# Kernel optimization log

Hardware: AMD Instinct MI355X
Metric: run time of the kernel (lower is better)

## Reference

```python
import jax, jax.numpy as jnp
import numpy as np

DIM = 512
HEAD_DIM = 32
NUM_HEADS = DIM // HEAD_DIM
SCALE = HEAD_DIM ** -0.5


def setup_inputs() -> dict:
    key = jax.random.key(0)
    k1, k2, k3 = jax.random.split(key, 3)
    B, H, W, C = 8, 32, 32, DIM
    x = jax.random.normal(k1, (B, H, W, C), dtype=jnp.float32)
    w_qkv = jax.random.normal(k2, (C, 3 * C), dtype=jnp.float32) * (C ** -0.5)
    w_proj = jax.random.normal(k3, (C, C), dtype=jnp.float32) * (C ** -0.5)
    b_proj = jnp.zeros((C,), dtype=jnp.float32)
    return {"x": x, "w_qkv": w_qkv, "w_proj": w_proj, "b_proj": b_proj}


def reference(x, w_qkv, w_proj, b_proj):
    B, H, W, C = x.shape
    N = H * W
    xt = x.reshape(B, N, C)
    qkv = xt @ w_qkv                       # [B, N, 3C]
    qkv = qkv.reshape(B, N, 3, NUM_HEADS, HEAD_DIM)
    qkv = jnp.transpose(qkv, (2, 0, 3, 1, 4))  # [3, B, heads, N, head_dim]
    q, k, v = qkv[0], qkv[1], qkv[2]
    attn = jnp.einsum('bhid,bhjd->bhij', q * SCALE, k)  # [B, heads, N, N]
    attn = jax.nn.softmax(attn, axis=-1)
    out = jnp.einsum('bhij,bhjd->bhid', attn, v)        # [B, heads, N, head_dim]
    out = jnp.transpose(out, (0, 2, 1, 3)).reshape(B, N, C)
    out = out @ w_proj + b_proj
    return out.reshape(B, H, W, C)
```

## Files before the change

### kernel.cpp

```cpp
#include <hip/hip_runtime.h>
#include <hip/hip_bf16.h>

typedef __bf16 bf16x8 __attribute__((ext_vector_type(8)));
typedef float  f32x4  __attribute__((ext_vector_type(4)));
typedef float  f32x16 __attribute__((ext_vector_type(16)));

#define NB 8
#define NTOK 1024
#define CDIM 512
#define NHEAD 16
#define HDIM 32
#define ATT_SCALE 0.17677669529663687f
#define LOG2E 1.4426950408889634f
#define QSCALE2 (ATT_SCALE * LOG2E)
#define NEGM2 (-12.0f * LOG2E)

struct __align__(8) bf4pack { __hip_bfloat16 x, y, z, w; };

__global__ __launch_bounds__(256)
void k_f32_to_bf16(const float* __restrict__ in, __hip_bfloat16* __restrict__ out, int n4) {
  int i = blockIdx.x * blockDim.x + threadIdx.x;
  if (i >= n4) return;
  float4 v = reinterpret_cast<const float4*>(in)[i];
  bf4pack o{__float2bfloat16(v.x), __float2bfloat16(v.y),
            __float2bfloat16(v.z), __float2bfloat16(v.w)};
  reinterpret_cast<bf4pack*>(out)[i] = o;
}

__global__ __launch_bounds__(256)
void k_transpose_bf16(const float* __restrict__ w, __hip_bfloat16* __restrict__ wt,
                      int K, int N) {
  __shared__ float tile[32][33];
  const int n0 = blockIdx.x * 32, k0 = blockIdx.y * 32;
  const int tx = threadIdx.x, ty = threadIdx.y;
  #pragma unroll
  for (int r = ty; r < 32; r += 8) tile[r][tx] = w[(size_t)(k0 + r) * N + n0 + tx];
  __syncthreads();
  #pragma unroll
  for (int r = ty; r < 32; r += 8)
    wt[(size_t)(n0 + r) * K + k0 + tx] = __float2bfloat16(tile[tx][r]);
}

__device__ __forceinline__ void gload_lds16(const void* g, void* l) {
  __builtin_amdgcn_global_load_lds(
      (const __attribute__((address_space(1))) unsigned int*)g,
      (__attribute__((address_space(3))) unsigned int*)l, 16, 0, 0);
}

template <int MODE>
__global__ __launch_bounds__(256, 2)
void gemm128(const __hip_bfloat16* __restrict__ A,
             const __hip_bfloat16* __restrict__ Bt,
             __hip_bfloat16* __restrict__ Qb,
             __hip_bfloat16* __restrict__ Kb,
             __hip_bfloat16* __restrict__ Vtb,
             float* __restrict__ outF,
             const float* __restrict__ bias,
             int mtiles, int ntiles) {
  __shared__ __hip_bfloat16 As[2][128 * 32];
  __shared__ __hip_bfloat16 Bs[2][128 * 32];

  const int t = threadIdx.x;
  const int wid = t >> 6, lane = t & 63;
  const int wr = wid >> 1, wc = wid & 1;
  const int lrow = lane & 15, lk8 = (lane >> 4) * 8;

  const int bid = blockIdx.x;
  const int chunk = (mtiles * ntiles) >> 3;
  const int wg = (bid & 7) * chunk + (bid >> 3);
  const int bm = (wg / ntiles) * 128;
  const int bn = (wg % ntiles) * 128;

  const bool swapped = (MODE == 0) && (bn >= 1024);

  const f32x4 fzero = {0.f, 0.f, 0.f, 0.f};
  f32x4 acc[4][4];
  #pragma unroll
  for (int m = 0; m < 4; ++m)
    #pragma unroll
    for (int n = 0; n < 4; ++n) acc[m][n] = fzero;

  auto stage = [&](int buf, int kt) {
    #pragma unroll
    for (int p = 0; p < 2; ++p) {
      const int c = p * 256 + t;
      const int row = c >> 2;
      const int kof = (c & 3) * 8;
      gload_lds16(A + (size_t)(bm + row) * CDIM + kt * 32 + kof,
                  &As[buf][(p * 256 + (t >> 6) * 64) * 8]);
      gload_lds16(Bt + (size_t)(bn + row) * CDIM + kt * 32 + kof,
                  &Bs[buf][(p * 256 + (t >> 6) * 64) * 8]);
    }
  };

  stage(0, 0);
  const int NKT = CDIM / 32;
  for (int kt = 0; kt < NKT; ++kt) {
    __syncthreads();
    if (kt + 1 < NKT) stage((kt + 1) & 1, kt + 1);
    const int bi = kt & 1;
    bf16x8 af[4], bfv[4];
    #pragma unroll
    for (int m = 0; m < 4; ++m)
      af[m] = *reinterpret_cast<const bf16x8*>(&As[bi][(wr * 64 + m * 16 + lrow) * 32 + lk8]);
    #pragma unroll
    for (int n = 0; n < 4; ++n)
      bfv[n] = *reinterpret_cast<const bf16x8*>(&Bs[bi][(wc * 64 + n * 16 + lrow) * 32 + lk8]);
    if (swapped) {
      #pragma unroll
      for (int m = 0; m < 4; ++m)
        #pragma unroll
        for (int n = 0; n < 4; ++n)
          acc[m][n] = __builtin_amdgcn_mfma_f32_16x16x32_bf16(bfv[n], af[m], acc[m][n], 0, 0, 0);
    } else {
      #pragma unroll
      for (int m = 0; m < 4; ++m)
        #pragma unroll
        for (int n = 0; n < 4; ++n)
          acc[m][n] = __builtin_amdgcn_mfma_f32_16x16x32_bf16(af[m], bfv[n], acc[m][n], 0, 0, 0);
    }
  }

  if constexpr (MODE == 0) {
    if (swapped) {
      #pragma unroll
      for (int m = 0; m < 4; ++m) {
        #pragma unroll
        for (int n = 0; n < 4; ++n) {
          #pragma unroll
          for (int i = 0; i < 4; ++i) {
            const int gn = bn + wc * 64 + n * 16 + (lane >> 4) * 4 + i;
            const int gm = bm + wr * 64 + m * 16 + lrow;
            const int r = gn & 511;
            const int h = r >> 5, d = r & 31;
            const int b = gm >> 10, tok = gm & 1023;
            const int ph = b * NHEAD + h;
            Vtb[((size_t)ph * HDIM + d) * NTOK + tok] = __float2bfloat16(acc[m][n][i]);
          }
        }
      }
    } else {
      #pragma unroll
      for (int m = 0; m < 4; ++m) {
        #pragma unroll
        for (int n = 0; n < 4; ++n) {
          #pragma unroll
          for (int i = 0; i < 4; ++i) {
            const int gm = bm + wr * 64 + m * 16 + (lane >> 4) * 4 + i;
            const int gn = bn + wc * 64 + n * 16 + lrow;
            const float v = acc[m][n][i];
            const int which = gn >> 9;
            const int r = gn & 511;
            const int h = r >> 5, d = r & 31;
            const int b = gm >> 10, tok = gm & 1023;
            const int ph = b * NHEAD + h;
            if (which == 0)
              Qb[((size_t)ph * NTOK + tok) * HDIM + d] = __float2bfloat16(v * QSCALE2);
            else
              Kb[((size_t)ph * NTOK + tok) * HDIM + d] = __float2bfloat16(v);
          }
        }
      }
    }
  } else {
    #pragma unroll
    for (int m = 0; m < 4; ++m) {
      #pragma unroll
      for (int n = 0; n < 4; ++n) {
        #pragma unroll
        for (int i = 0; i < 4; ++i) {
          const int gm = bm + wr * 64 + m * 16 + (lane >> 4) * 4 + i;
          const int gn = bn + wc * 64 + n * 16 + lrow;
          outF[(size_t)gm * CDIM + gn] = acc[m][n][i] + bias[gn];
        }
      }
    }
  }
}

__device__ __forceinline__ unsigned pk2(float a, float b) {
  union { __hip_bfloat16 h; unsigned short u; } x, y;
  x.h = __float2bfloat16(a); y.h = __float2bfloat16(b);
  return (unsigned)x.u | ((unsigned)y.u << 16);
}

union B32x4 { unsigned u[4]; bf16x8 v; };

__global__ __launch_bounds__(256)
void k_attn(const __hip_bfloat16* __restrict__ Q,
            const __hip_bfloat16* __restrict__ K,
            const __hip_bfloat16* __restrict__ Vt,
            __hip_bfloat16* __restrict__ out) {
  const int wid = threadIdx.x >> 6, lane = threadIdx.x & 63;
  const int pair = blockIdx.x & 127;
  const int qblk = blockIdx.x >> 7;
  const int b = pair >> 4, h = pair & 15;
  const int q0 = qblk * 128 + wid * 32;
  const int lq = lane & 31, hi = lane >> 5;

  const size_t pb = (size_t)pair * NTOK * HDIM;
  const bf16x8 qf0 = *reinterpret_cast<const bf16x8*>(&Q[pb + (size_t)(q0 + lq) * HDIM + hi * 8]);
  const bf16x8 qf1 = *reinterpret_cast<const bf16x8*>(&Q[pb + (size_t)(q0 + lq) * HDIM + 16 + hi * 8]);

  f32x16 o;
  #pragma unroll
  for (int r = 0; r < 16; ++r) o[r] = 0.f;
  float l_r = 0.f;

  const __hip_bfloat16* Kp = &K[pb + (size_t)lq * HDIM + hi * 8];
  const __hip_bfloat16* Vp = &Vt[(size_t)pair * HDIM * NTOK + (size_t)lq * NTOK + hi * 8];

  for (int t = 0; t < 32; ++t) {
    const __hip_bfloat16* kb = Kp + (size_t)t * 32 * HDIM;
    const bf16x8 kf0 = *reinterpret_cast<const bf16x8*>(kb);
    const bf16x8 kf1 = *reinterpret_cast<const bf16x8*>(kb + 16);
    f32x16 s;
    #pragma unroll
    for (int r = 0; r < 16; ++r) s[r] = NEGM2;
    s = __builtin_amdgcn_mfma_f32_32x32x16_bf16(kf0, qf0, s, 0, 0, 0);
    s = __builtin_amdgcn_mfma_f32_32x32x16_bf16(kf1, qf1, s, 0, 0, 0);

    float p[16];
    float ts = 0.f;
    #pragma unroll
    for (int r = 0; r < 16; ++r) { p[r] = __builtin_amdgcn_exp2f(s[r]); ts += p[r]; }
    ts += __shfl_xor(ts, 32, 64);
    l_r += ts;

    #pragma unroll
    for (int ks = 0; ks < 2; ++ks) {
      const int r0 = 8 * ks;
      const bf16x8 vf = *reinterpret_cast<const bf16x8*>(Vp + t * 32 + ks * 16);
      const unsigned pA = pk2(p[r0 + 0], p[r0 + 1]);
      const unsigned pB = pk2(p[r0 + 2], p[r0 + 3]);
      const unsigned pC = pk2(p[r0 + 4], p[r0 + 5]);
      const unsigned pD = pk2(p[r0 + 6], p[r0 + 7]);
      const unsigned sA = hi ? pA : pC;
      const unsigned sB = hi ? pB : pD;
      const unsigned rA = (unsigned)__shfl_xor((int)sA, 32, 64);
      const unsigned rB = (unsigned)__shfl_xor((int)sB, 32, 64);
      B32x4 f;
      f.u[0] = hi ? rA : pA;
      f.u[1] = hi ? rB : pB;
      f.u[2] = hi ? pC : rA;
      f.u[3] = hi ? pD : rB;
      o = __builtin_amdgcn_mfma_f32_32x32x16_bf16(vf, f.v, o, 0, 0, 0);
    }
  }

  const float rinv = 1.0f / l_r;
  __hip_bfloat16* orow = &out[((size_t)b * NTOK + q0 + lq) * CDIM + h * HDIM];
  #pragma unroll
  for (int g = 0; g < 4; ++g) {
    bf4pack w;
    w.x = __float2bfloat16(o[4 * g + 0] * rinv);
    w.y = __float2bfloat16(o[4 * g + 1] * rinv);
    w.z = __float2bfloat16(o[4 * g + 2] * rinv);
    w.w = __float2bfloat16(o[4 * g + 3] * rinv);
    *reinterpret_cast<bf4pack*>(orow + 8 * g + 4 * hi) = w;
  }
}

extern "C" void kernel_launch(void* const* d_in, const int* in_sizes, int n_in,
                              void* d_out, int out_size, void* d_ws, size_t ws_size,
                              hipStream_t stream) {
  (void)in_sizes; (void)n_in; (void)out_size; (void)ws_size;
  const float* x      = (const float*)d_in[0];
  const float* w_qkv  = (const float*)d_in[1];
  const float* w_proj = (const float*)d_in[2];
  const float* b_proj = (const float*)d_in[3];
  float* out = (float*)d_out;

  char* ws = (char*)d_ws;
  __hip_bfloat16* xb     = (__hip_bfloat16*)(ws);
  __hip_bfloat16* attnO  = xb;
  __hip_bfloat16* wqkvT  = (__hip_bfloat16*)(ws + 8388608);
  __hip_bfloat16* wprojT = (__hip_bfloat16*)(ws + 9961472);
  __hip_bfloat16* Qb     = (__hip_bfloat16*)(ws + 10485760);
  __hip_bfloat16* Kb     = (__hip_bfloat16*)(ws + 18874368);
  __hip_bfloat16* Vtb    = (__hip_bfloat16*)(ws + 27262976);

  k_f32_to_bf16<<<4096, 256, 0, stream>>>(x, xb, (NB * NTOK * CDIM) / 4);
  k_transpose_bf16<<<dim3(1536 / 32, 512 / 32), dim3(32, 8), 0, stream>>>(w_qkv, wqkvT, 512, 1536);
  k_transpose_bf16<<<dim3(512 / 32, 512 / 32), dim3(32, 8), 0, stream>>>(w_proj, wprojT, 512, 512);

  gemm128<0><<<64 * 12, 256, 0, stream>>>(xb, wqkvT, Qb, Kb, Vtb, nullptr, nullptr, 64, 12);
  k_attn<<<128 * 8, 256, 0, stream>>>(Qb, Kb, Vtb, attnO);
  gemm128<1><<<64 * 4, 256, 0, stream>>>(attnO, wprojT, nullptr, nullptr, nullptr, out, b_proj, 64, 4);
}
```

Measured before the change: 165.4 us.

## Vectorize GEMM epilogue stores, prefetch K, use permlane swap in attention

The GEMM epilogue now picks the MFMA operand order per output target, so each lane holds four contiguous elements. That lets Q/K, Vt and the fp32 output be written as packed 4-wide stores instead of scalar scattered stores, with the bias loaded as float4. The attention kernel prefetches the next K tile one iteration ahead and loads both V fragments early. It replaces the shuffle-based P repacking with v_permlane32_swap, defers the cross-half row-sum reduction to the end, and sets an occupancy hint of 4. Bf16 conversion uses native __bf16 vector casts. The prefetch adds register pressure, and the occupancy hint could force spills.

Measured after the change: 169.0 us. 1.02x slower.

```diff
diff --git a/kernel.cpp b/kernel.cpp
--- a/kernel.cpp
+++ b/kernel.cpp
@@ -2,6 +2,8 @@
 #include <hip/hip_bf16.h>
 
 typedef __bf16 bf16x8 __attribute__((ext_vector_type(8)));
+typedef __bf16 bf16x4v __attribute__((ext_vector_type(4)));
+typedef __bf16 bf16x2v __attribute__((ext_vector_type(2)));
 typedef float  f32x4  __attribute__((ext_vector_type(4)));
 typedef float  f32x16 __attribute__((ext_vector_type(16)));
 
@@ -22,9 +24,8 @@
   int i = blockIdx.x * blockDim.x + threadIdx.x;
   if (i >= n4) return;
   float4 v = reinterpret_cast<const float4*>(in)[i];
-  bf4pack o{__float2bfloat16(v.x), __float2bfloat16(v.y),
-            __float2bfloat16(v.z), __float2bfloat16(v.w)};
-  reinterpret_cast<bf4pack*>(out)[i] = o;
+  bf16x4v o = {(__bf16)v.x, (__bf16)v.y, (__bf16)v.z, (__bf16)v.w};
+  reinterpret_cast<bf16x4v*>(out)[i] = o;
 }
 
 __global__ __launch_bounds__(256)
@@ -71,7 +72,7 @@
   const int bm = (wg / ntiles) * 128;
   const int bn = (wg % ntiles) * 128;
 
-  const bool swapped = (MODE == 0) && (bn >= 1024);
+  const bool swapped = (MODE == 1) || (bn < 1024);
 
   const f32x4 fzero = {0.f, 0.f, 0.f, 0.f};
   f32x4 acc[4][4];
@@ -123,20 +124,21 @@
 
   if constexpr (MODE == 0) {
     if (swapped) {
+      const float sc = (bn < 512) ? QSCALE2 : 1.0f;
+      __hip_bfloat16* dst = (bn < 512) ? Qb : Kb;
       #pragma unroll
       for (int m = 0; m < 4; ++m) {
         #pragma unroll
         for (int n = 0; n < 4; ++n) {
-          #pragma unroll
-          for (int i = 0; i < 4; ++i) {
-            const int gn = bn + wc * 64 + n * 16 + (lane >> 4) * 4 + i;
-            const int gm = bm + wr * 64 + m * 16 + lrow;
-            const int r = gn & 511;
-            const int h = r >> 5, d = r & 31;
-            const int b = gm >> 10, tok = gm & 1023;
-            const int ph = b * NHEAD + h;
-            Vtb[((size_t)ph * HDIM + d) * NTOK + tok] = __float2bfloat16(acc[m][n][i]);
-          }
+          const int gm = bm + wr * 64 + m * 16 + lrow;
+          const int gn0 = bn + wc * 64 + n * 16 + (lane >> 4) * 4;
+          const int r = gn0 & 511;
+          const int hh = r >> 5, d0 = r & 31;
+          const int bb = gm >> 10, tok = gm & 1023;
+          const int ph = bb * NHEAD + hh;
+          bf16x4v pk = {(__bf16)(acc[m][n][0] * sc), (__bf16)(acc[m][n][1] * sc),
+                        (__bf16)(acc[m][n][2] * sc), (__bf16)(acc[m][n][3] * sc)};
+          *reinterpret_cast<bf16x4v*>(&dst[((size_t)ph * NTOK + tok) * HDIM + d0]) = pk;
         }
       }
     } else {
@@ -144,49 +146,48 @@
       for (int m = 0; m < 4; ++m) {
         #pragma unroll
         for (int n = 0; n < 4; ++n) {
-          #pragma unroll
-          for (int i = 0; i < 4; ++i) {
-            const int gm = bm + wr * 64 + m * 16 + (lane >> 4) * 4 + i;
-            const int gn = bn + wc * 64 + n * 16 + lrow;
-            const float v = acc[m][n][i];
-            const int which = gn >> 9;
-            const int r = gn & 511;
-            const int h = r >> 5, d = r & 31;
-            const int b = gm >> 10, tok = gm & 1023;
-            const int ph = b * NHEAD + h;
-            if (which == 0)
-              Qb[((size_t)ph * NTOK + tok) * HDIM + d] = __float2bfloat16(v * QSCALE2);
-            else
-              Kb[((size_t)ph * NTOK + tok) * HDIM + d] = __float2bfloat16(v);
-          }
+          const int gm0 = bm + wr * 64 + m * 16 + (lane >> 4) * 4;
+          const int gn = bn + wc * 64 + n * 16 + lrow;
+          const int r = gn & 511;
+          const int hh = r >> 5, d = r & 31;
+          const int bb = gm0 >> 10, tok0 = gm0 & 1023;
+          const int ph = bb * NHEAD + hh;
+          bf16x4v pk = {(__bf16)acc[m][n][0], (__bf16)acc[m][n][1],
+                        (__bf16)acc[m][n][2], (__bf16)acc[m][n][3]};
+          *reinterpret_cast<bf16x4v*>(&Vtb[((size_t)ph * HDIM + d) * NTOK + tok0]) = pk;
         }
       }
     }
   } else {
+    float4 bias4[4];
+    #pragma unroll
+    for (int n = 0; n < 4; ++n)
+      bias4[n] = *reinterpret_cast<const float4*>(&bias[bn + wc * 64 + n * 16 + (lane >> 4) * 4]);
     #pragma unroll
     for (int m = 0; m < 4; ++m) {
       #pragma unroll
       for (int n = 0; n < 4; ++n) {
-        #pragma unroll
-        for (int i = 0; i < 4; ++i) {
-          const int gm = bm + wr * 64 + m * 16 + (lane >> 4) * 4 + i;
-          const int gn = bn + wc * 64 + n * 16 + lrow;
-          outF[(size_t)gm * CDIM + gn] = acc[m][n][i] + bias[gn];
-        }
+        const int gm = bm + wr * 64 + m * 16 + lrow;
+        const int gn0 = bn + wc * 64 + n * 16 + (lane >> 4) * 4;
+        float4 w;
+        w.x = acc[m][n][0] + bias4[n].x;
+        w.y = acc[m][n][1] + bias4[n].y;
+        w.z = acc[m][n][2] + bias4[n].z;
+        w.w = acc[m][n][3] + bias4[n].w;
+        *reinterpret_cast<float4*>(&outF[(size_t)gm * CDIM + gn0]) = w;
       }
     }
   }
 }
 
 __device__ __forceinline__ unsigned pk2(float a, float b) {
-  union { __hip_bfloat16 h; unsigned short u; } x, y;
-  x.h = __float2bfloat16(a); y.h = __float2bfloat16(b);
-  return (unsigned)x.u | ((unsigned)y.u << 16);
+  bf16x2v t = {(__bf16)a, (__bf16)b};
+  return __builtin_bit_cast(unsigned, t);
 }
 
 union B32x4 { unsigned u[4]; bf16x8 v; };
 
-__global__ __launch_bounds__(256)
+__global__ __launch_bounds__(256, 4)
 void k_attn(const __hip_bfloat16* __restrict__ Q,
             const __hip_bfloat16* __restrict__ K,
             const __hip_bfloat16* __restrict__ Vt,
@@ -210,54 +211,59 @@
   const __hip_bfloat16* Kp = &K[pb + (size_t)lq * HDIM + hi * 8];
   const __hip_bfloat16* Vp = &Vt[(size_t)pair * HDIM * NTOK + (size_t)lq * NTOK + hi * 8];
 
+  bf16x8 kc0 = *reinterpret_cast<const bf16x8*>(Kp);
+  bf16x8 kc1 = *reinterpret_cast<const bf16x8*>(Kp + 16);
+
   for (int t = 0; t < 32; ++t) {
-    const __hip_bfloat16* kb = Kp + (size_t)t * 32 * HDIM;
-    const bf16x8 kf0 = *reinterpret_cast<const bf16x8*>(kb);
-    const bf16x8 kf1 = *reinterpret_cast<const bf16x8*>(kb + 16);
+    const int tn = (t < 31) ? t + 1 : 31;
+    const bf16x8 kn0 = *reinterpret_cast<const bf16x8*>(Kp + (size_t)tn * 32 * HDIM);
+    const bf16x8 kn1 = *reinterpret_cast<const bf16x8*>(Kp + (size_t)tn * 32 * HDIM + 16);
+    const bf16x8 vf0 = *reinterpret_cast<const bf16x8*>(Vp + t * 32);
+    const bf16x8 vf1 = *reinterpret_cast<const bf16x8*>(Vp + t * 32 + 16);
+
     f32x16 s;
     #pragma unroll
     for (int r = 0; r < 16; ++r) s[r] = NEGM2;
-    s = __builtin_amdgcn_mfma_f32_32x32x16_bf16(kf0, qf0, s, 0, 0, 0);
-    s = __builtin_amdgcn_mfma_f32_32x32x16_bf16(kf1, qf1, s, 0, 0, 0);
+    s = __builtin_amdgcn_mfma_f32_32x32x16_bf16(kc0, qf0, s, 0, 0, 0);
+    s = __builtin_amdgcn_mfma_f32_32x32x16_bf16(kc1, qf1, s, 0, 0, 0);
 
     float p[16];
-    float ts = 0.f;
-    #pragma unroll
-    for (int r = 0; r < 16; ++r) { p[r] = __builtin_amdgcn_exp2f(s[r]); ts += p[r]; }
-    ts += __shfl_xor(ts, 32, 64);
-    l_r += ts;
-
-    #pragma unroll
-    for (int ks = 0; ks < 2; ++ks) {
-      const int r0 = 8 * ks;
-      const bf16x8 vf = *reinterpret_cast<const bf16x8*>(Vp + t * 32 + ks * 16);
-      const unsigned pA = pk2(p[r0 + 0], p[r0 + 1]);
-      const unsigned pB = pk2(p[r0 + 2], p[r0 + 3]);
-      const unsigned pC = pk2(p[r0 + 4], p[r0 + 5]);
-      const unsigned pD = pk2(p[r0 + 6], p[r0 + 7]);
-      const unsigned sA = hi ? pA : pC;
-      const unsigned sB = hi ? pB : pD;
-      const unsigned rA = (unsigned)__shfl_xor((int)sA, 32, 64);
-      const unsigned rB = (unsigned)__shfl_xor((int)sB, 32, 64);
-      B32x4 f;
-      f.u[0] = hi ? rA : pA;
-      f.u[1] = hi ? rB : pB;
-      f.u[2] = hi ? pC : rA;
-      f.u[3] = hi ? pD : rB;
-      o = __builtin_amdgcn_mfma_f32_32x32x16_bf16(vf, f.v, o, 0, 0, 0);
-    }
-  }
-
+    #pragma unroll
+    for (int r = 0; r < 16; ++r) p[r] = __builtin_amdgcn_exp2f(s[r]);
+    {
+      const float a0 = p[0] + p[1], a1 = p[2] + p[3], a2 = p[4] + p[5], a3 = p[6] + p[7];
+      const float a4 = p[8] + p[9], a5 = p[10] + p[11], a6 = p[12] + p[13], a7 = p[14] + p[15];
+      const float b0 = a0 + a1, b1 = a2 + a3, b2 = a4 + a5, b3 = a6 + a7;
+      l_r += (b0 + b1) + (b2 + b3);
+    }
+
+    {
+      unsigned pA = pk2(p[0], p[1]), pB = pk2(p[2], p[3]);
+      unsigned pC = pk2(p[4], p[5]), pD = pk2(p[6], p[7]);
+      asm("v_permlane32_swap_b32 %0, %1" : "+v"(pA), "+v"(pC));
+      asm("v_permlane32_swap_b32 %0, %1" : "+v"(pB), "+v"(pD));
+      B32x4 f; f.u[0] = pA; f.u[1] = pB; f.u[2] = pC; f.u[3] = pD;
+      o = __builtin_amdgcn_mfma_f32_32x32x16_bf16(vf0, f.v, o, 0, 0, 0);
+    }
+    {
+      unsigned pA = pk2(p[8], p[9]), pB = pk2(p[10], p[11]);
+      unsigned pC = pk2(p[12], p[13]), pD = pk2(p[14], p[15]);
+      asm("v_permlane32_swap_b32 %0, %1" : "+v"(pA), "+v"(pC));
+      asm("v_permlane32_swap_b32 %0, %1" : "+v"(pB), "+v"(pD));
+      B32x4 f; f.u[0] = pA; f.u[1] = pB; f.u[2] = pC; f.u[3] = pD;
+      o = __builtin_amdgcn_mfma_f32_32x32x16_bf16(vf1, f.v, o, 0, 0, 0);
+    }
+    kc0 = kn0; kc1 = kn1;
+  }
+
+  l_r += __shfl_xor(l_r, 32, 64);
   const float rinv = 1.0f / l_r;
   __hip_bfloat16* orow = &out[((size_t)b * NTOK + q0 + lq) * CDIM + h * HDIM];
   #pragma unroll
   for (int g = 0; g < 4; ++g) {
-    bf4pack w;
-    w.x = __float2bfloat16(o[4 * g + 0] * rinv);
-    w.y = __float2bfloat16(o[4 * g + 1] * rinv);
-    w.z = __float2bfloat16(o[4 * g + 2] * rinv);
-    w.w = __float2bfloat16(o[4 * g + 3] * rinv);
-    *reinterpret_cast<bf4pack*>(orow + 8 * g + 4 * hi) = w;
+    bf16x4v w = {(__bf16)(o[4 * g + 0] * rinv), (__bf16)(o[4 * g + 1] * rinv),
+                 (__bf16)(o[4 * g + 2] * rinv), (__bf16)(o[4 * g + 3] * rinv)};
+    *reinterpret_cast<bf16x4v*>(orow + 8 * g + 4 * hi) = w;
   }
 }
 
```
